# Kernel tuning notes

Measured on AMD Instinct MI355X. Metric: run time of the kernel, lower is better.

The kernel has to match this reference:

```python
import jax, jax.numpy as jnp
import numpy as np

E = 1024
H = 16
D = E // H  # head_dim = 64
FF = 4 * E
EPS = 1e-5


def layernorm(x, g, b):
    mu = jnp.mean(x, axis=-1, keepdims=True)
    var = jnp.var(x, axis=-1, keepdims=True)
    return (x - mu) * jax.lax.rsqrt(var + EPS) * g + b


def setup_inputs() -> dict:
    key = jax.random.key(0)
    ks = jax.random.split(key, 12)
    s = 1.0 / np.sqrt(E)
    sf = 1.0 / np.sqrt(FF)
    return {
        "x": jax.random.normal(ks[0], (2, 2048, E), dtype=jnp.float32),
        "wq": jax.random.uniform(ks[1], (E, E), jnp.float32, -s, s),
        "wk": jax.random.uniform(ks[2], (E, E), jnp.float32, -s, s),
        "wv": jax.random.uniform(ks[3], (E, E), jnp.float32, -s, s),
        "wo": jax.random.uniform(ks[4], (E, E), jnp.float32, -s, s),
        "bo": jax.random.uniform(ks[5], (E,), jnp.float32, -s, s),
        "g1": jnp.ones((E,), jnp.float32),
        "b1": jnp.zeros((E,), jnp.float32),
        "w1": jax.random.uniform(ks[6], (FF, E), jnp.float32, -s, s),
        "bf1": jax.random.uniform(ks[7], (FF,), jnp.float32, -s, s),
        "w2": jax.random.uniform(ks[8], (E, FF), jnp.float32, -sf, sf),
        "bf2": jax.random.uniform(ks[9], (E,), jnp.float32, -sf, sf),
        "g2": jnp.ones((E,), jnp.float32),
        "b2": jnp.zeros((E,), jnp.float32),
    }


def reference(x, wq, wk, wv, wo, bo, g1, b1, w1, bf1, w2, bf2, g2, b2):
    B, L, _ = x.shape
    # projections (torch Linear: x @ W.T)
    q = (x @ wq.T).reshape(B, L, H, D).transpose(0, 2, 1, 3)  # (B,H,L,D)
    k = (x @ wk.T).reshape(B, L, H, D).transpose(0, 2, 1, 3)
    v = (x @ wv.T).reshape(B, L, H, D).transpose(0, 2, 1, 3)
    scores = jnp.einsum('bhqd,bhkd->bhqk', q, k) / np.sqrt(D)
    attn = jax.nn.softmax(scores, axis=-1)
    ctx = jnp.einsum('bhqk,bhkd->bhqd', attn, v)
    ctx = ctx.transpose(0, 2, 1, 3).reshape(B, L, E)
    attn_out = ctx @ wo.T + bo
    h = layernorm(x + attn_out, g1, b1)
    ff = jax.nn.gelu(h @ w1.T + bf1, approximate=False) @ w2.T + bf2
    return layernorm(h + ff, g2, b2)
```

## Files before the change

kernel.cpp:

```cpp
#include <hip/hip_runtime.h>
#include <hip/hip_bf16.h>
#include <stdint.h>

typedef __bf16 bf16x8 __attribute__((ext_vector_type(8)));
typedef float  f32x4  __attribute__((ext_vector_type(4)));
typedef unsigned short u16;
typedef u16 u16x8 __attribute__((ext_vector_type(8)));

__device__ __forceinline__ u16 f2b(float f) {
  uint32_t u = __builtin_bit_cast(uint32_t, f);
  u += 0x7fffu + ((u >> 16) & 1u);
  return (u16)(u >> 16);
}

__device__ __forceinline__ float b2f(u16 b) {
  uint32_t u = (uint32_t)b << 16;
  return __builtin_bit_cast(float, u);
}

__device__ __forceinline__ f32x4 mfma16(bf16x8 a, bf16x8 b, f32x4 c) {
  return __builtin_amdgcn_mfma_f32_16x16x32_bf16(a, b, c, 0, 0, 0);
}

__device__ __forceinline__ void gload_lds16(const void* g, void* l) {
  __builtin_amdgcn_global_load_lds(
      (const __attribute__((address_space(1))) void*)g,
      (__attribute__((address_space(3))) void*)l, 16, 0, 0);
}

__global__ void f2b_all(const float* __restrict__ x,  const float* __restrict__ wq,
                        const float* __restrict__ wk, const float* __restrict__ wv,
                        const float* __restrict__ wo, const float* __restrict__ w1,
                        const float* __restrict__ w2,
                        u16* __restrict__ xb, u16* __restrict__ wqkvb,
                        u16* __restrict__ wob, u16* __restrict__ w1b,
                        u16* __restrict__ w2b) {
  const int i = blockIdx.x * blockDim.x + threadIdx.x;
  const float* src; u16* dst; int off;
  if (i < 524288)        { src = x;  dst = xb;              off = i; }
  else if (i < 655360)   { src = wq; dst = wqkvb;           off = i - 524288; }
  else if (i < 786432)   { src = wk; dst = wqkvb + 1048576; off = i - 655360; }
  else if (i < 917504)   { src = wv; dst = wqkvb + 2097152; off = i - 786432; }
  else if (i < 1048576)  { src = wo; dst = wob;             off = i - 917504; }
  else if (i < 1572864)  { src = w1; dst = w1b;             off = i - 1048576; }
  else                   { src = w2; dst = w2b;             off = i - 1572864; }
  const float4* p = (const float4*)src + (size_t)off * 2;
  float4 a = p[0], b = p[1];
  u16x8 r;
  r[0] = f2b(a.x); r[1] = f2b(a.y); r[2] = f2b(a.z); r[3] = f2b(a.w);
  r[4] = f2b(b.x); r[5] = f2b(b.y); r[6] = f2b(b.z); r[7] = f2b(b.w);
  *((u16x8*)dst + off) = r;
}

template<int MODE>
__global__ __launch_bounds__(256, 4) void gemm_bt(
    const u16* __restrict__ A, const u16* __restrict__ W,
    const float* __restrict__ bias,
    void* __restrict__ o0, void* __restrict__ o1,
    void* __restrict__ o2, void* __restrict__ o3,
    int Nsz, int Kstride, int Klen, int ntiles)
{
  __shared__ u16 As[2][128 * 32];
  __shared__ u16 Bs[2][128 * 32];
  const int nbn = Nsz >> 7;
  int bid = blockIdx.x;
  bid = (bid & 7) * ((int)gridDim.x >> 3) + (bid >> 3);
  const int tile = (MODE == 1) ? (bid % ntiles) : bid;
  const int sid  = (MODE == 1) ? (bid / ntiles) : 0;
  const int koff = sid * Klen;
  const int bm = tile / nbn;
  const int bn = tile % nbn;
  const int tid = threadIdx.x;
  const int w = tid >> 6, l = tid & 63;
  const int lh = l >> 4, ll = l & 15;
  const int wr = w >> 1, wc = w & 1;

  f32x4 acc[4][4] = {};

  const u16* Ag = A + (size_t)(bm * 128) * Kstride + koff;
  const u16* Wg = W + (size_t)(bn * 128) * Kstride + koff;

  const int flat0 = (w * 2) * 64 + l;
  const int flat1 = (w * 2 + 1) * 64 + l;

  {
    gload_lds16(Ag + (size_t)(flat0 >> 2) * Kstride + (flat0 & 3) * 8, As[0] + flat0 * 8);
    gload_lds16(Wg + (size_t)(flat0 >> 2) * Kstride + (flat0 & 3) * 8, Bs[0] + flat0 * 8);
    gload_lds16(Ag + (size_t)(flat1 >> 2) * Kstride + (flat1 & 3) * 8, As[0] + flat1 * 8);
    gload_lds16(Wg + (size_t)(flat1 >> 2) * Kstride + (flat1 & 3) * 8, Bs[0] + flat1 * 8);
  }
  __syncthreads();

  const int NS = Klen >> 5;
  int buf = 0;
  for (int s = 0; s < NS; ++s) {
    if (s + 1 < NS) {
      const int k0 = (s + 1) * 32;
      gload_lds16(Ag + (size_t)(flat0 >> 2) * Kstride + k0 + (flat0 & 3) * 8, As[buf ^ 1] + flat0 * 8);
      gload_lds16(Wg + (size_t)(flat0 >> 2) * Kstride + k0 + (flat0 & 3) * 8, Bs[buf ^ 1] + flat0 * 8);
      gload_lds16(Ag + (size_t)(flat1 >> 2) * Kstride + k0 + (flat1 & 3) * 8, As[buf ^ 1] + flat1 * 8);
      gload_lds16(Wg + (size_t)(flat1 >> 2) * Kstride + k0 + (flat1 & 3) * 8, Bs[buf ^ 1] + flat1 * 8);
    }
    bf16x8 af[4], bfr[4];
#pragma unroll
    for (int mi = 0; mi < 4; ++mi)
      af[mi] = *(const bf16x8*)(As[buf] + (wr * 64 + mi * 16 + ll) * 32 + lh * 8);
#pragma unroll
    for (int ni = 0; ni < 4; ++ni)
      bfr[ni] = *(const bf16x8*)(Bs[buf] + (wc * 64 + ni * 16 + ll) * 32 + lh * 8);
    __builtin_amdgcn_s_setprio(1);
#pragma unroll
    for (int mi = 0; mi < 4; ++mi)
#pragma unroll
      for (int ni = 0; ni < 4; ++ni)
        acc[mi][ni] = mfma16(af[mi], bfr[ni], acc[mi][ni]);
    __builtin_amdgcn_s_setprio(0);
    __syncthreads();
    buf ^= 1;
  }

#pragma unroll
  for (int mi = 0; mi < 4; ++mi) {
#pragma unroll
    for (int ni = 0; ni < 4; ++ni) {
      const int col = bn * 128 + wc * 64 + ni * 16 + ll;
#pragma unroll
      for (int i = 0; i < 4; ++i) {
        const int row = bm * 128 + wr * 64 + mi * 16 + lh * 4 + i;
        float v = acc[mi][ni][i];
        if (MODE == 1) {
          u16* dst = (sid == 0) ? (u16*)o0 : (sid == 1) ? (u16*)o1
                   : (sid == 2) ? (u16*)o2 : (u16*)o3;
          dst[(size_t)row * Nsz + col] = f2b(v);
        } else if (MODE == 2) {
          float xx = v + bias[col];
          float u = xx * (0.7978845608f + 0.0356774081f * xx * xx);
          float t = __builtin_amdgcn_exp2f(u * 2.8853900818f);
          float r = __builtin_amdgcn_rcpf(1.0f + t);
          ((u16*)o0)[(size_t)row * Nsz + col] = f2b(xx * t * r);
        } else {
          const int which = col >> 10;
          const int e = col & 1023;
          const int hh = e >> 6, dd = e & 63;
          const int bb = row >> 11, nl = row & 2047;
          if (which == 0) {
            ((u16*)o0)[((size_t)(bb * 16 + hh) * 2048 + nl) * 64 + dd] = f2b(v * 0.18033688f);
          } else if (which == 1) {
            ((u16*)o1)[((size_t)(bb * 16 + hh) * 2048 + nl) * 64 + dd] = f2b(v);
          } else {
            ((u16*)o2)[((size_t)(bb * 16 + hh) * 64 + dd) * 2048 + nl] = f2b(v);
          }
        }
      }
    }
  }
}

__global__ __launch_bounds__(256, 3) void attn_fwd(
    const u16* __restrict__ Q, const u16* __restrict__ K,
    const u16* __restrict__ Vt, u16* __restrict__ ctx)
{
  __shared__ u16 Ks[2][64 * 64];
  __shared__ u16 Vs[2][64 * 64];
  __shared__ u16 Ps[4][32 * 64];

  const int bh = blockIdx.x & 31;
  const int qt = blockIdx.x >> 5;
  const int tid = threadIdx.x;
  const int w = tid >> 6, l = tid & 63;
  const int lh = l >> 4, ll = l & 15;
  const int q0 = qt * 128 + w * 32;

  bf16x8 qf[2][2];
#pragma unroll
  for (int qh = 0; qh < 2; ++qh) {
    const u16* Qg = Q + ((size_t)bh * 2048 + q0 + qh * 16 + ll) * 64;
#pragma unroll
    for (int kk = 0; kk < 2; ++kk)
      qf[qh][kk] = *(const bf16x8*)(Qg + kk * 32 + lh * 8);
  }

  bf16x8 ones;
  {
    const u16 o = 0x3F80;
#pragma unroll
    for (int i = 0; i < 8; ++i) ones[i] = __builtin_bit_cast(__bf16, o);
  }

  f32x4 cacc[2][4] = {};
  f32x4 lacc[2] = {};
  u16* ps = Ps[w];

  const int f0 = tid, f1 = 256 + tid;
  const int r0 = f0 >> 3, s0 = f0 & 7, g0 = (s0 ^ (r0 & 7)) * 8;
  const int r1 = f1 >> 3, s1 = f1 & 7, g1 = (s1 ^ (r1 & 7)) * 8;

  {
    gload_lds16(K + ((size_t)bh * 2048 + r0) * 64 + g0, Ks[0] + f0 * 8);
    gload_lds16(Vt + ((size_t)bh * 64 + r0) * 2048 + g0, Vs[0] + f0 * 8);
    gload_lds16(K + ((size_t)bh * 2048 + r1) * 64 + g1, Ks[0] + f1 * 8);
    gload_lds16(Vt + ((size_t)bh * 64 + r1) * 2048 + g1, Vs[0] + f1 * 8);
  }
  __syncthreads();

  for (int kt = 0; kt < 32; ++kt) {
    const int b = kt & 1;
    if (kt < 31) {
      const int kn = (kt + 1) * 64;
      gload_lds16(K + ((size_t)bh * 2048 + kn + r0) * 64 + g0, Ks[b ^ 1] + f0 * 8);
      gload_lds16(Vt + ((size_t)bh * 64 + r0) * 2048 + kn + g0, Vs[b ^ 1] + f0 * 8);
      gload_lds16(K + ((size_t)bh * 2048 + kn + r1) * 64 + g1, Ks[b ^ 1] + f1 * 8);
      gload_lds16(Vt + ((size_t)bh * 64 + r1) * 2048 + kn + g1, Vs[b ^ 1] + f1 * 8);
    }

    f32x4 st[2][4];
    __builtin_amdgcn_s_setprio(1);
#pragma unroll
    for (int jb = 0; jb < 4; ++jb) {
      f32x4 a0 = {}, a1 = {};
#pragma unroll
      for (int kk = 0; kk < 2; ++kk) {
        const int r = jb * 16 + ll;
        bf16x8 kf = *(const bf16x8*)(Ks[b] + r * 64 + (((kk * 4 + lh) ^ (r & 7)) * 8));
        a0 = mfma16(kf, qf[0][kk], a0);
        a1 = mfma16(kf, qf[1][kk], a1);
      }
      st[0][jb] = a0; st[1][jb] = a1;
    }
    __builtin_amdgcn_s_setprio(0);

#pragma unroll
    for (int qh = 0; qh < 2; ++qh)
#pragma unroll
      for (int jb = 0; jb < 4; ++jb) {
        const float p0 = __builtin_amdgcn_exp2f(st[qh][jb][0]);
        const float p1 = __builtin_amdgcn_exp2f(st[qh][jb][1]);
        const float p2 = __builtin_amdgcn_exp2f(st[qh][jb][2]);
        const float p3 = __builtin_amdgcn_exp2f(st[qh][jb][3]);
        uint2 pk;
        asm("v_cvt_pk_bf16_f32 %0, %1, %2" : "=v"(pk.x) : "v"(p0), "v"(p1));
        asm("v_cvt_pk_bf16_f32 %0, %1, %2" : "=v"(pk.y) : "v"(p2), "v"(p3));
        *(uint2*)(ps + (qh * 16 + ll) * 64 +
                  (((jb * 2 + (lh >> 1)) ^ (ll & 7)) * 8) + (lh & 1) * 4) = pk;
      }

    asm volatile("s_waitcnt lgkmcnt(0)" ::: "memory");
    __builtin_amdgcn_sched_barrier(0);

    __builtin_amdgcn_s_setprio(1);
#pragma unroll
    for (int kk = 0; kk < 2; ++kk) {
      bf16x8 pf0 = *(const bf16x8*)(ps + ll * 64 + (((kk * 4 + lh) ^ (ll & 7)) * 8));
      bf16x8 pf1 = *(const bf16x8*)(ps + (16 + ll) * 64 + (((kk * 4 + lh) ^ (ll & 7)) * 8));
      lacc[0] = mfma16(pf0, ones, lacc[0]);
      lacc[1] = mfma16(pf1, ones, lacc[1]);
#pragma unroll
      for (int db = 0; db < 4; ++db) {
        const int vr = db * 16 + ll;
        bf16x8 vf = *(const bf16x8*)(Vs[b] + vr * 64 + (((kk * 4 + lh) ^ (vr & 7)) * 8));
        cacc[0][db] = mfma16(pf0, vf, cacc[0][db]);
        cacc[1][db] = mfma16(pf1, vf, cacc[1][db]);
      }
    }
    __builtin_amdgcn_s_setprio(0);
    __syncthreads();
  }

  const int bb = bh >> 4, hh = bh & 15;
#pragma unroll
  for (int qh = 0; qh < 2; ++qh)
#pragma unroll
    for (int db = 0; db < 4; ++db)
#pragma unroll
      for (int i = 0; i < 4; ++i) {
        const float v = cacc[qh][db][i] / lacc[qh][i];
        const size_t orow = (size_t)bb * 2048 + q0 + qh * 16 + lh * 4 + i;
        const size_t ocol = (size_t)hh * 64 + db * 16 + ll;
        ctx[orow * 1024 + ocol] = f2b(v);
      }
}

__global__ __launch_bounds__(256) void ln_fused(
    const float* __restrict__ a,  const u16* __restrict__ p0,
    const u16* __restrict__ p1,   const u16* __restrict__ p2,
    const u16* __restrict__ p3,   const float* __restrict__ bias,
    const float* __restrict__ g,  const float* __restrict__ be,
    float* __restrict__ ho, u16* __restrict__ hb)
{
  const int row = blockIdx.x;
  const int t = threadIdx.x;
  const size_t base = (size_t)row * 1024 + t * 4;
  float4 xa = *(const float4*)(a + base);
  float v0 = xa.x, v1 = xa.y, v2 = xa.z, v3 = xa.w;
  {
    ushort4 c = *(const ushort4*)(p0 + base);
    v0 += b2f(c.x); v1 += b2f(c.y); v2 += b2f(c.z); v3 += b2f(c.w);
  }
  if (p1) {
    ushort4 c = *(const ushort4*)(p1 + base);
    v0 += b2f(c.x); v1 += b2f(c.y); v2 += b2f(c.z); v3 += b2f(c.w);
  }
  if (p2) {
    ushort4 c = *(const ushort4*)(p2 + base);
    v0 += b2f(c.x); v1 += b2f(c.y); v2 += b2f(c.z); v3 += b2f(c.w);
  }
  if (p3) {
    ushort4 c = *(const ushort4*)(p3 + base);
    v0 += b2f(c.x); v1 += b2f(c.y); v2 += b2f(c.z); v3 += b2f(c.w);
  }
  if (bias) {
    float4 xd = *(const float4*)(bias + t * 4);
    v0 += xd.x; v1 += xd.y; v2 += xd.z; v3 += xd.w;
  }
  float s = v0 + v1 + v2 + v3;
  float ss = v0 * v0 + v1 * v1 + v2 * v2 + v3 * v3;
#pragma unroll
  for (int d = 1; d < 64; d <<= 1) {
    s += __shfl_xor(s, d);
    ss += __shfl_xor(ss, d);
  }
  __shared__ float red[8];
  const int w = t >> 6, lid = t & 63;
  if (lid == 0) { red[w] = s; red[4 + w] = ss; }
  __syncthreads();
  s = red[0] + red[1] + red[2] + red[3];
  ss = red[4] + red[5] + red[6] + red[7];
  const float mean = s * (1.0f / 1024.0f);
  const float var = ss * (1.0f / 1024.0f) - mean * mean;
  const float rstd = rsqrtf(var + 1e-5f);
  const float vv[4] = {v0, v1, v2, v3};
#pragma unroll
  for (int i = 0; i < 4; ++i) {
    const int col = t * 4 + i;
    const float hv = (vv[i] - mean) * rstd * g[col] + be[col];
    if (ho) ho[base + i] = hv;
    if (hb) hb[base + i] = f2b(hv);
  }
}

extern "C" void kernel_launch(void* const* d_in, const int* in_sizes, int n_in,
                              void* d_out, int out_size, void* d_ws, size_t ws_size,
                              hipStream_t stream) {
  const float* x   = (const float*)d_in[0];
  const float* wq  = (const float*)d_in[1];
  const float* wk  = (const float*)d_in[2];
  const float* wv  = (const float*)d_in[3];
  const float* wo  = (const float*)d_in[4];
  const float* bo  = (const float*)d_in[5];
  const float* g1  = (const float*)d_in[6];
  const float* b1  = (const float*)d_in[7];
  const float* w1  = (const float*)d_in[8];
  const float* bf1 = (const float*)d_in[9];
  const float* w2  = (const float*)d_in[10];
  const float* bf2 = (const float*)d_in[11];
  const float* g2  = (const float*)d_in[12];
  const float* b2  = (const float*)d_in[13];

  char* ws = (char*)d_ws;
  const size_t MB = 1u << 20;
  u16* xb    = (u16*)(ws + 0);
  u16* wqkv  = (u16*)(ws + 8 * MB);
  u16* wob   = (u16*)(ws + 14 * MB);
  u16* w1b   = (u16*)(ws + 16 * MB);
  u16* w2b   = (u16*)(ws + 24 * MB);
  u16* qb    = (u16*)(ws + 32 * MB);
  u16* kb    = (u16*)(ws + 40 * MB);
  u16* vtb   = (u16*)(ws + 48 * MB);
  u16* ctxb  = (u16*)(ws + 56 * MB);
  u16* sp0   = (u16*)(ws + 64 * MB);
  u16* sp1   = (u16*)(ws + 72 * MB);
  u16* sp2   = (u16*)(ws + 0);
  u16* sp3   = (u16*)(ws + 8 * MB);
  float* hbuf = (float*)(ws + 80 * MB);
  u16* hbb   = (u16*)(ws + 96 * MB);
  u16* ff1   = (u16*)(ws + 32 * MB);

  f2b_all<<<8192, 256, 0, stream>>>(x, wq, wk, wv, wo, w1, w2, xb, wqkv, wob, w1b, w2b);

  gemm_bt<0><<<768, 256, 0, stream>>>(xb, wqkv, nullptr, qb, kb, vtb, nullptr,
                                      3072, 1024, 1024, 768);
  attn_fwd<<<512, 256, 0, stream>>>(qb, kb, vtb, ctxb);
  gemm_bt<1><<<1024, 256, 0, stream>>>(ctxb, wob, nullptr, sp0, sp1, sp2, sp3,
                                       1024, 1024, 256, 256);
  ln_fused<<<4096, 256, 0, stream>>>(x, sp0, sp1, sp2, sp3, bo, g1, b1, hbuf, hbb);
  gemm_bt<2><<<1024, 256, 0, stream>>>(hbb, w1b, bf1, ff1, nullptr, nullptr, nullptr,
                                       4096, 1024, 1024, 1024);
  gemm_bt<1><<<1024, 256, 0, stream>>>(ff1, w2b, nullptr, sp0, sp1, sp2, sp3,
                                       1024, 4096, 1024, 256);
  ln_fused<<<4096, 256, 0, stream>>>(hbuf, sp0, sp1, sp2, sp3, bf2, g2, b2,
                                     (float*)d_out, nullptr);
}
```

Measured before the change: 246.1 us.

## Triple-buffer attention K/V tiles and read bf16 residuals in layernorm

Attention now keeps three K/V LDS stages, prefetching two tiles ahead and using explicit vmcnt waits plus s_barrier instead of __syncthreads, with launch bounds lowered to 2 blocks per CU. Layernorm kernels read the residual from bf16 copies (xb, hbb) instead of fp32 x and an fp32 h buffer, dropping the fp32 h write. Split-K scratch buffers are relocated so they no longer alias xb. This trades occupancy and residual precision for deeper load overlap and less memory traffic.

```diff
diff --git a/kernel.cpp b/kernel.cpp
--- a/kernel.cpp
+++ b/kernel.cpp
@@ -156,12 +156,12 @@
   }
 }
 
-__global__ __launch_bounds__(256, 3) void attn_fwd(
+__global__ __launch_bounds__(256, 2) void attn_fwd(
     const u16* __restrict__ Q, const u16* __restrict__ K,
     const u16* __restrict__ Vt, u16* __restrict__ ctx)
 {
-  __shared__ u16 Ks[2][64 * 64];
-  __shared__ u16 Vs[2][64 * 64];
+  __shared__ u16 Ks[3][64 * 64];
+  __shared__ u16 Vs[3][64 * 64];
   __shared__ u16 Ps[4][32 * 64];
 
   const int bh = blockIdx.x & 31;
@@ -195,23 +195,22 @@
   const int r0 = f0 >> 3, s0 = f0 & 7, g0 = (s0 ^ (r0 & 7)) * 8;
   const int r1 = f1 >> 3, s1 = f1 & 7, g1 = (s1 ^ (r1 & 7)) * 8;
 
-  {
-    gload_lds16(K + ((size_t)bh * 2048 + r0) * 64 + g0, Ks[0] + f0 * 8);
-    gload_lds16(Vt + ((size_t)bh * 64 + r0) * 2048 + g0, Vs[0] + f0 * 8);
-    gload_lds16(K + ((size_t)bh * 2048 + r1) * 64 + g1, Ks[0] + f1 * 8);
-    gload_lds16(Vt + ((size_t)bh * 64 + r1) * 2048 + g1, Vs[0] + f1 * 8);
-  }
-  __syncthreads();
+  auto stage = [&](int t) {
+    const int b = t % 3;
+    const int kn = t * 64;
+    gload_lds16(K + ((size_t)bh * 2048 + kn + r0) * 64 + g0, Ks[b] + f0 * 8);
+    gload_lds16(Vt + ((size_t)bh * 64 + r0) * 2048 + kn + g0, Vs[b] + f0 * 8);
+    gload_lds16(K + ((size_t)bh * 2048 + kn + r1) * 64 + g1, Ks[b] + f1 * 8);
+    gload_lds16(Vt + ((size_t)bh * 64 + r1) * 2048 + kn + g1, Vs[b] + f1 * 8);
+  };
+
+  stage(0); stage(1);
+  asm volatile("s_waitcnt vmcnt(4) lgkmcnt(0)" ::: "memory");
+  asm volatile("s_barrier" ::: "memory");
 
   for (int kt = 0; kt < 32; ++kt) {
-    const int b = kt & 1;
-    if (kt < 31) {
-      const int kn = (kt + 1) * 64;
-      gload_lds16(K + ((size_t)bh * 2048 + kn + r0) * 64 + g0, Ks[b ^ 1] + f0 * 8);
-      gload_lds16(Vt + ((size_t)bh * 64 + r0) * 2048 + kn + g0, Vs[b ^ 1] + f0 * 8);
-      gload_lds16(K + ((size_t)bh * 2048 + kn + r1) * 64 + g1, Ks[b ^ 1] + f1 * 8);
-      gload_lds16(Vt + ((size_t)bh * 64 + r1) * 2048 + kn + g1, Vs[b ^ 1] + f1 * 8);
-    }
+    const int b = kt % 3;
+    if (kt < 30) stage(kt + 2);
 
     f32x4 st[2][4];
     __builtin_amdgcn_s_setprio(1);
@@ -263,7 +262,9 @@
       }
     }
     __builtin_amdgcn_s_setprio(0);
-    __syncthreads();
+    if (kt < 30) asm volatile("s_waitcnt vmcnt(4) lgkmcnt(0)" ::: "memory");
+    else         asm volatile("s_waitcnt vmcnt(0) lgkmcnt(0)" ::: "memory");
+    asm volatile("s_barrier" ::: "memory");
   }
 
   const int bb = bh >> 4, hh = bh & 15;
@@ -281,17 +282,20 @@
 }
 
 __global__ __launch_bounds__(256) void ln_fused(
-    const float* __restrict__ a,  const u16* __restrict__ p0,
-    const u16* __restrict__ p1,   const u16* __restrict__ p2,
-    const u16* __restrict__ p3,   const float* __restrict__ bias,
-    const float* __restrict__ g,  const float* __restrict__ be,
-    float* __restrict__ ho, u16* __restrict__ hb)
+    const u16* __restrict__ res, const u16* __restrict__ p0,
+    const u16* __restrict__ p1,  const u16* __restrict__ p2,
+    const u16* __restrict__ p3,  const float* __restrict__ bias,
+    const float* __restrict__ g, const float* __restrict__ be,
+    float* __restrict__ fo, u16* __restrict__ bo16)
 {
   const int row = blockIdx.x;
   const int t = threadIdx.x;
   const size_t base = (size_t)row * 1024 + t * 4;
-  float4 xa = *(const float4*)(a + base);
-  float v0 = xa.x, v1 = xa.y, v2 = xa.z, v3 = xa.w;
+  float v0, v1, v2, v3;
+  {
+    ushort4 c = *(const ushort4*)(res + base);
+    v0 = b2f(c.x); v1 = b2f(c.y); v2 = b2f(c.z); v3 = b2f(c.w);
+  }
   {
     ushort4 c = *(const ushort4*)(p0 + base);
     v0 += b2f(c.x); v1 += b2f(c.y); v2 += b2f(c.z); v3 += b2f(c.w);
@@ -333,8 +337,8 @@
   for (int i = 0; i < 4; ++i) {
     const int col = t * 4 + i;
     const float hv = (vv[i] - mean) * rstd * g[col] + be[col];
-    if (ho) ho[base + i] = hv;
-    if (hb) hb[base + i] = f2b(hv);
+    if (fo) fo[base + i] = hv;
+    if (bo16) bo16[base + i] = f2b(hv);
   }
 }
 
@@ -369,9 +373,8 @@
   u16* ctxb  = (u16*)(ws + 56 * MB);
   u16* sp0   = (u16*)(ws + 64 * MB);
   u16* sp1   = (u16*)(ws + 72 * MB);
-  u16* sp2   = (u16*)(ws + 0);
-  u16* sp3   = (u16*)(ws + 8 * MB);
-  float* hbuf = (float*)(ws + 80 * MB);
+  u16* sp2   = (u16*)(ws + 80 * MB);
+  u16* sp3   = (u16*)(ws + 88 * MB);
   u16* hbb   = (u16*)(ws + 96 * MB);
   u16* ff1   = (u16*)(ws + 32 * MB);
 
@@ -382,11 +385,12 @@
   attn_fwd<<<512, 256, 0, stream>>>(qb, kb, vtb, ctxb);
   gemm_bt<1><<<1024, 256, 0, stream>>>(ctxb, wob, nullptr, sp0, sp1, sp2, sp3,
                                        1024, 1024, 256, 256);
-  ln_fused<<<4096, 256, 0, stream>>>(x, sp0, sp1, sp2, sp3, bo, g1, b1, hbuf, hbb);
+  ln_fused<<<4096, 256, 0, stream>>>(xb, sp0, sp1, sp2, sp3, bo, g1, b1,
+                                     nullptr, hbb);
   gemm_bt<2><<<1024, 256, 0, stream>>>(hbb, w1b, bf1, ff1, nullptr, nullptr, nullptr,
                                        4096, 1024, 1024, 1024);
   gemm_bt<1><<<1024, 256, 0, stream>>>(ff1, w2b, nullptr, sp0, sp1, sp2, sp3,
                                        1024, 4096, 1024, 256);
-  ln_fused<<<4096, 256, 0, stream>>>(hbuf, sp0, sp1, sp2, sp3, bf2, g2, b2,
+  ln_fused<<<4096, 256, 0, stream>>>(hbb, sp0, sp1, sp2, sp3, bf2, g2, b2,
                                      (float*)d_out, nullptr);
 }
```

Measured after the change: 242.8 us. Within noise of the previous version (-1.3%).

## Switch GEMM to 32x32x16 MFMA with XOR-swizzled LDS and bf16 residuals

Applied to the files above, without the earlier changes.

The GEMM inner loop now uses 32x32x16 bf16 MFMA instructions with 2x2 accumulator tiles per wave instead of 4x4 tiles of 16x16x32. It also XOR-swizzles the k-chunk placement in LDS to reduce bank conflicts on fragment reads. The layernorm kernels now read the residual as bf16 (xb and hbb) instead of fp32 and drop the fp32 hidden-state buffer, which cuts memory traffic. In exchange the residual path loses precision, and the split-K partial buffers move to dedicated workspace regions.

```diff
diff --git a/kernel.cpp b/kernel.cpp
--- a/kernel.cpp
+++ b/kernel.cpp
@@ -4,6 +4,7 @@
 
 typedef __bf16 bf16x8 __attribute__((ext_vector_type(8)));
 typedef float  f32x4  __attribute__((ext_vector_type(4)));
+typedef float  f32x16 __attribute__((ext_vector_type(16)));
 typedef unsigned short u16;
 typedef u16 u16x8 __attribute__((ext_vector_type(8)));
 
@@ -20,6 +21,10 @@
 
 __device__ __forceinline__ f32x4 mfma16(bf16x8 a, bf16x8 b, f32x4 c) {
   return __builtin_amdgcn_mfma_f32_16x16x32_bf16(a, b, c, 0, 0, 0);
+}
+
+__device__ __forceinline__ f32x16 mfma32(bf16x8 a, bf16x8 b, f32x16 c) {
+  return __builtin_amdgcn_mfma_f32_32x32x16_bf16(a, b, c, 0, 0, 0);
 }
 
 __device__ __forceinline__ void gload_lds16(const void* g, void* l) {
@@ -72,22 +77,24 @@
   const int bn = tile % nbn;
   const int tid = threadIdx.x;
   const int w = tid >> 6, l = tid & 63;
-  const int lh = l >> 4, ll = l & 15;
+  const int lo5 = l & 31, hi = l >> 5;
   const int wr = w >> 1, wc = w & 1;
 
-  f32x4 acc[4][4] = {};
+  f32x16 acc[2][2] = {};
 
   const u16* Ag = A + (size_t)(bm * 128) * Kstride + koff;
   const u16* Wg = W + (size_t)(bn * 128) * Kstride + koff;
 
   const int flat0 = (w * 2) * 64 + l;
   const int flat1 = (w * 2 + 1) * 64 + l;
+  const int r0 = flat0 >> 2, sl0 = flat0 & 3, gs0 = (sl0 ^ (r0 & 3)) * 8;
+  const int r1 = flat1 >> 2, sl1 = flat1 & 3, gs1 = (sl1 ^ (r1 & 3)) * 8;
 
   {
-    gload_lds16(Ag + (size_t)(flat0 >> 2) * Kstride + (flat0 & 3) * 8, As[0] + flat0 * 8);
-    gload_lds16(Wg + (size_t)(flat0 >> 2) * Kstride + (flat0 & 3) * 8, Bs[0] + flat0 * 8);
-    gload_lds16(Ag + (size_t)(flat1 >> 2) * Kstride + (flat1 & 3) * 8, As[0] + flat1 * 8);
-    gload_lds16(Wg + (size_t)(flat1 >> 2) * Kstride + (flat1 & 3) * 8, Bs[0] + flat1 * 8);
+    gload_lds16(Ag + (size_t)r0 * Kstride + gs0, As[0] + flat0 * 8);
+    gload_lds16(Wg + (size_t)r0 * Kstride + gs0, Bs[0] + flat0 * 8);
+    gload_lds16(Ag + (size_t)r1 * Kstride + gs1, As[0] + flat1 * 8);
+    gload_lds16(Wg + (size_t)r1 * Kstride + gs1, Bs[0] + flat1 * 8);
   }
   __syncthreads();
 
@@ -96,38 +103,43 @@
   for (int s = 0; s < NS; ++s) {
     if (s + 1 < NS) {
       const int k0 = (s + 1) * 32;
-      gload_lds16(Ag + (size_t)(flat0 >> 2) * Kstride + k0 + (flat0 & 3) * 8, As[buf ^ 1] + flat0 * 8);
-      gload_lds16(Wg + (size_t)(flat0 >> 2) * Kstride + k0 + (flat0 & 3) * 8, Bs[buf ^ 1] + flat0 * 8);
-      gload_lds16(Ag + (size_t)(flat1 >> 2) * Kstride + k0 + (flat1 & 3) * 8, As[buf ^ 1] + flat1 * 8);
-      gload_lds16(Wg + (size_t)(flat1 >> 2) * Kstride + k0 + (flat1 & 3) * 8, Bs[buf ^ 1] + flat1 * 8);
+      gload_lds16(Ag + (size_t)r0 * Kstride + k0 + gs0, As[buf ^ 1] + flat0 * 8);
+      gload_lds16(Wg + (size_t)r0 * Kstride + k0 + gs0, Bs[buf ^ 1] + flat0 * 8);
+      gload_lds16(Ag + (size_t)r1 * Kstride + k0 + gs1, As[buf ^ 1] + flat1 * 8);
+      gload_lds16(Wg + (size_t)r1 * Kstride + k0 + gs1, Bs[buf ^ 1] + flat1 * 8);
     }
-    bf16x8 af[4], bfr[4];
-#pragma unroll
-    for (int mi = 0; mi < 4; ++mi)
-      af[mi] = *(const bf16x8*)(As[buf] + (wr * 64 + mi * 16 + ll) * 32 + lh * 8);
-#pragma unroll
-    for (int ni = 0; ni < 4; ++ni)
-      bfr[ni] = *(const bf16x8*)(Bs[buf] + (wc * 64 + ni * 16 + ll) * 32 + lh * 8);
+    bf16x8 af[2][2], bfr[2][2];
+#pragma unroll
+    for (int kk = 0; kk < 2; ++kk)
+#pragma unroll
+      for (int mi = 0; mi < 2; ++mi) {
+        const int rA = wr * 64 + mi * 32 + lo5;
+        af[kk][mi] = *(const bf16x8*)(As[buf] + rA * 32 + (((kk * 2 + hi) ^ (rA & 3)) * 8));
+        const int rB = wc * 64 + mi * 32 + lo5;
+        bfr[kk][mi] = *(const bf16x8*)(Bs[buf] + rB * 32 + (((kk * 2 + hi) ^ (rB & 3)) * 8));
+      }
     __builtin_amdgcn_s_setprio(1);
 #pragma unroll
-    for (int mi = 0; mi < 4; ++mi)
-#pragma unroll
-      for (int ni = 0; ni < 4; ++ni)
-        acc[mi][ni] = mfma16(af[mi], bfr[ni], acc[mi][ni]);
+    for (int kk = 0; kk < 2; ++kk)
+#pragma unroll
+      for (int mi = 0; mi < 2; ++mi)
+#pragma unroll
+        for (int ni = 0; ni < 2; ++ni)
+          acc[mi][ni] = mfma32(af[kk][mi], bfr[kk][ni], acc[mi][ni]);
     __builtin_amdgcn_s_setprio(0);
     __syncthreads();
     buf ^= 1;
   }
 
 #pragma unroll
-  for (int mi = 0; mi < 4; ++mi) {
-#pragma unroll
-    for (int ni = 0; ni < 4; ++ni) {
-      const int col = bn * 128 + wc * 64 + ni * 16 + ll;
-#pragma unroll
-      for (int i = 0; i < 4; ++i) {
-        const int row = bm * 128 + wr * 64 + mi * 16 + lh * 4 + i;
-        float v = acc[mi][ni][i];
+  for (int mi = 0; mi < 2; ++mi) {
+#pragma unroll
+    for (int ni = 0; ni < 2; ++ni) {
+      const int col = bn * 128 + wc * 64 + ni * 32 + lo5;
+#pragma unroll
+      for (int r = 0; r < 16; ++r) {
+        const int row = bm * 128 + wr * 64 + mi * 32 + hi * 4 + (r & 3) + 8 * (r >> 2);
+        float v = acc[mi][ni][r];
         if (MODE == 1) {
           u16* dst = (sid == 0) ? (u16*)o0 : (sid == 1) ? (u16*)o1
                    : (sid == 2) ? (u16*)o2 : (u16*)o3;
@@ -136,8 +148,8 @@
           float xx = v + bias[col];
           float u = xx * (0.7978845608f + 0.0356774081f * xx * xx);
           float t = __builtin_amdgcn_exp2f(u * 2.8853900818f);
-          float r = __builtin_amdgcn_rcpf(1.0f + t);
-          ((u16*)o0)[(size_t)row * Nsz + col] = f2b(xx * t * r);
+          float rc = __builtin_amdgcn_rcpf(1.0f + t);
+          ((u16*)o0)[(size_t)row * Nsz + col] = f2b(xx * t * rc);
         } else {
           const int which = col >> 10;
           const int e = col & 1023;
@@ -281,17 +293,20 @@
 }
 
 __global__ __launch_bounds__(256) void ln_fused(
-    const float* __restrict__ a,  const u16* __restrict__ p0,
-    const u16* __restrict__ p1,   const u16* __restrict__ p2,
-    const u16* __restrict__ p3,   const float* __restrict__ bias,
-    const float* __restrict__ g,  const float* __restrict__ be,
-    float* __restrict__ ho, u16* __restrict__ hb)
+    const u16* __restrict__ res, const u16* __restrict__ p0,
+    const u16* __restrict__ p1,  const u16* __restrict__ p2,
+    const u16* __restrict__ p3,  const float* __restrict__ bias,
+    const float* __restrict__ g, const float* __restrict__ be,
+    float* __restrict__ fo, u16* __restrict__ bo16)
 {
   const int row = blockIdx.x;
   const int t = threadIdx.x;
   const size_t base = (size_t)row * 1024 + t * 4;
-  float4 xa = *(const float4*)(a + base);
-  float v0 = xa.x, v1 = xa.y, v2 = xa.z, v3 = xa.w;
+  float v0, v1, v2, v3;
+  {
+    ushort4 c = *(const ushort4*)(res + base);
+    v0 = b2f(c.x); v1 = b2f(c.y); v2 = b2f(c.z); v3 = b2f(c.w);
+  }
   {
     ushort4 c = *(const ushort4*)(p0 + base);
     v0 += b2f(c.x); v1 += b2f(c.y); v2 += b2f(c.z); v3 += b2f(c.w);
@@ -333,8 +348,8 @@
   for (int i = 0; i < 4; ++i) {
     const int col = t * 4 + i;
     const float hv = (vv[i] - mean) * rstd * g[col] + be[col];
-    if (ho) ho[base + i] = hv;
-    if (hb) hb[base + i] = f2b(hv);
+    if (fo) fo[base + i] = hv;
+    if (bo16) bo16[base + i] = f2b(hv);
   }
 }
 
@@ -369,9 +384,8 @@
   u16* ctxb  = (u16*)(ws + 56 * MB);
   u16* sp0   = (u16*)(ws + 64 * MB);
   u16* sp1   = (u16*)(ws + 72 * MB);
-  u16* sp2   = (u16*)(ws + 0);
-  u16* sp3   = (u16*)(ws + 8 * MB);
-  float* hbuf = (float*)(ws + 80 * MB);
+  u16* sp2   = (u16*)(ws + 80 * MB);
+  u16* sp3   = (u16*)(ws + 88 * MB);
   u16* hbb   = (u16*)(ws + 96 * MB);
   u16* ff1   = (u16*)(ws + 32 * MB);
 
@@ -382,11 +396,12 @@
   attn_fwd<<<512, 256, 0, stream>>>(qb, kb, vtb, ctxb);
   gemm_bt<1><<<1024, 256, 0, stream>>>(ctxb, wob, nullptr, sp0, sp1, sp2, sp3,
                                        1024, 1024, 256, 256);
-  ln_fused<<<4096, 256, 0, stream>>>(x, sp0, sp1, sp2, sp3, bo, g1, b1, hbuf, hbb);
+  ln_fused<<<4096, 256, 0, stream>>>(xb, sp0, sp1, sp2, sp3, bo, g1, b1,
+                                     nullptr, hbb);
   gemm_bt<2><<<1024, 256, 0, stream>>>(hbb, w1b, bf1, ff1, nullptr, nullptr, nullptr,
                                        4096, 1024, 1024, 1024);
   gemm_bt<1><<<1024, 256, 0, stream>>>(ff1, w2b, nullptr, sp0, sp1, sp2, sp3,
                                        1024, 4096, 1024, 256);
-  ln_fused<<<4096, 256, 0, stream>>>(hbuf, sp0, sp1, sp2, sp3, bf2, g2, b2,
+  ln_fused<<<4096, 256, 0, stream>>>(hbb, sp0, sp1, sp2, sp3, bf2, g2, b2,
                                      (float*)d_out, nullptr);
 }
```

Result: slower. 270.9 us (+10.1%).
